# Kernel tuning notes

Measured on AMD Instinct MI355X. Metric: run time of the kernel, lower is better.

Reference implementation:

```python
import jax, jax.numpy as jnp
import numpy as np

N = 100000   # nodes
E = 600000   # edges per sign
IN = 128     # in_dim
HID = 128    # hidden_dim
H = 8        # num_heads
D = HID // H # per-head out_feats = 16
OUT = 64     # out_dim
NEG_SLOPE = 0.2


def setup_inputs() -> dict:
    key = jax.random.key(0)
    ks = jax.random.split(key, 20)
    inp = {}
    inp['features'] = jax.random.normal(ks[0], (N, IN), dtype=jnp.float32)
    inp['pos_src'] = jax.random.randint(ks[1], (E,), 0, N, dtype=jnp.int32)
    inp['pos_dst'] = jax.random.randint(ks[2], (E,), 0, N, dtype=jnp.int32)
    inp['neg_src'] = jax.random.randint(ks[3], (E,), 0, N, dtype=jnp.int32)
    inp['neg_dst'] = jax.random.randint(ks[4], (E,), 0, N, dtype=jnp.int32)
    # GATConv params (DGL: fc weight, attn_l, attn_r, bias) for pos and neg convs
    s = 0.1
    inp['W_pos'] = jax.random.normal(ks[5], (IN, H * D), dtype=jnp.float32) * s
    inp['al_pos'] = jax.random.normal(ks[6], (H, D), dtype=jnp.float32) * s
    inp['ar_pos'] = jax.random.normal(ks[7], (H, D), dtype=jnp.float32) * s
    inp['b_pos'] = jnp.zeros((H * D,), dtype=jnp.float32)
    inp['W_neg'] = jax.random.normal(ks[8], (IN, H * D), dtype=jnp.float32) * s
    inp['al_neg'] = jax.random.normal(ks[9], (H, D), dtype=jnp.float32) * s
    inp['ar_neg'] = jax.random.normal(ks[10], (H, D), dtype=jnp.float32) * s
    inp['b_neg'] = jnp.zeros((H * D,), dtype=jnp.float32)
    # final MLP: Linear(2*HID, HID) -> ReLU -> Linear(HID, OUT)
    inp['W1'] = jax.random.normal(ks[11], (2 * HID, HID), dtype=jnp.float32) * s
    inp['b1'] = jnp.zeros((HID,), dtype=jnp.float32)
    inp['W2'] = jax.random.normal(ks[12], (HID, OUT), dtype=jnp.float32) * s
    inp['b2'] = jnp.zeros((OUT,), dtype=jnp.float32)
    return inp


def gat_conv(features, src, dst, W, al, ar, b, n):
    # DGL GATConv (eval mode, no feat/attn dropout, no residual/activation)
    feat = (features @ W).reshape(n, H, D)            # [N,H,D]
    el = (feat * al).sum(-1)                          # [N,H]
    er = (feat * ar).sum(-1)                          # [N,H]
    e = jax.nn.leaky_relu(el[src] + er[dst], NEG_SLOPE)  # [E,H] per-edge logits
    # edge softmax over incoming edges of each dst node, per head
    m = jax.ops.segment_max(e, dst, num_segments=n)   # [N,H]
    ex = jnp.exp(e - m[dst])                          # [E,H]
    s = jax.ops.segment_sum(ex, dst, num_segments=n)  # [N,H]
    a = ex / s[dst]                                   # [E,H]
    rst = jax.ops.segment_sum(a[:, :, None] * feat[src], dst, num_segments=n)  # [N,H,D]
    return rst.reshape(n, H * D) + b


def reference(features, pos_src, pos_dst, neg_src, neg_dst,
              W_pos, al_pos, ar_pos, b_pos,
              W_neg, al_neg, ar_neg, b_neg,
              W1, b1, W2, b2):
    n = features.shape[0]
    h_pos = gat_conv(features, pos_src, pos_dst, W_pos, al_pos, ar_pos, b_pos, n)
    h_neg = gat_conv(features, neg_src, neg_dst, W_neg, al_neg, ar_neg, b_neg, n)
    h = jnp.concatenate([h_pos, h_neg], axis=1)       # [N, 2*HID]
    h_final = jnp.maximum(h @ W1 + b1, 0.0) @ W2 + b2  # [N, OUT]
    return (h_pos, h_neg, h_final)
```

## Files before the change

kernel.cpp:

```cpp
#include <hip/hip_runtime.h>

#define NEG_SLOPE 0.2f

typedef __attribute__((ext_vector_type(8))) short short8;
typedef __attribute__((ext_vector_type(4))) float floatx4;

__device__ __forceinline__ unsigned short f2bf(float f) {
    union { float f; unsigned u; } v; v.f = f;
    unsigned r = v.u + 0x7FFF + ((v.u >> 16) & 1);
    return (unsigned short)(r >> 16);
}
__device__ __forceinline__ float bf2f(unsigned short u) {
    return __uint_as_float(((unsigned)u) << 16);
}

__global__ void convert_w_kernel(const float* __restrict__ Wp, const float* __restrict__ Wn,
                                 const float* __restrict__ W1, const float* __restrict__ W2,
                                 unsigned short* __restrict__ Wcat, unsigned short* __restrict__ W1t,
                                 unsigned short* __restrict__ W2t) {
    int i = blockIdx.x * blockDim.x + threadIdx.x;
    if (i < 256 * 128) {
        int nr = i >> 7, k = i & 127;
        float v = (nr < 128) ? Wp[k * 128 + nr] : Wn[k * 128 + (nr - 128)];
        Wcat[i] = f2bf(v);
    } else if (i < 256 * 128 + 128 * 256) {
        int j = i - 256 * 128;
        int nr = j >> 8, k = j & 255;
        W1t[j] = f2bf(W1[k * 128 + nr]);
    } else if (i < 256 * 128 + 128 * 256 + 64 * 128) {
        int j = i - 256 * 128 - 128 * 256;
        int nr = j >> 7, k = j & 127;
        W2t[j] = f2bf(W2[k * 64 + nr]);
    }
}

template<int KDIM, int BN, bool IN_F32, bool RELU, bool OUT_BF16>
__global__ __launch_bounds__(256)
void mfma_gemm_kernel(const void* __restrict__ Av, const unsigned short* __restrict__ Wt,
                      const float* __restrict__ bias, void* __restrict__ outv, int n_rows) {
    constexpr int BM = 128, BK = 64;
    constexpr int LDA = BK + 8;
    constexpr int NT = BN / 32;
    __shared__ unsigned short As[BM * LDA];
    __shared__ unsigned short Bs[BN * LDA];
    const int tid = threadIdx.x;
    const int lane = tid & 63;
    const int wave = tid >> 6;
    const int wy = wave >> 1, wx = wave & 1;
    const int row0 = blockIdx.x * BM;
    const int n0 = blockIdx.y * BN;
    const int lrow = lane & 15;
    const int lk = (lane >> 4) * 8;

    floatx4 acc[4][NT];
#pragma unroll
    for (int mt = 0; mt < 4; mt++)
#pragma unroll
        for (int nt = 0; nt < NT; nt++) acc[mt][nt] = (floatx4){0.f, 0.f, 0.f, 0.f};

    for (int kb = 0; kb < KDIM / BK; ++kb) {
#pragma unroll
        for (int u = 0; u < 4; ++u) {
            int idx = tid + u * 256;
            int r = idx >> 3, c8 = idx & 7;
            int gr = row0 + r; if (gr >= n_rows) gr = n_rows - 1;
            if (IN_F32) {
                const float* Af = (const float*)Av + (size_t)gr * KDIM + kb * BK + c8 * 8;
                float4 va = ((const float4*)Af)[0], vb = ((const float4*)Af)[1];
                unsigned short o[8];
                o[0] = f2bf(va.x); o[1] = f2bf(va.y); o[2] = f2bf(va.z); o[3] = f2bf(va.w);
                o[4] = f2bf(vb.x); o[5] = f2bf(vb.y); o[6] = f2bf(vb.z); o[7] = f2bf(vb.w);
                *(float4*)&As[r * LDA + c8 * 8] = *(float4*)o;
            } else {
                const unsigned short* Ab = (const unsigned short*)Av;
                float4 v = *(const float4*)(Ab + (size_t)gr * KDIM + kb * BK + c8 * 8);
                *(float4*)&As[r * LDA + c8 * 8] = v;
            }
        }
#pragma unroll
        for (int u = 0; u < BN / 32; ++u) {
            int idx = tid + u * 256;
            int r = idx >> 3, c8 = idx & 7;
            float4 v = *(const float4*)(Wt + (size_t)(n0 + r) * KDIM + kb * BK + c8 * 8);
            *(float4*)&Bs[r * LDA + c8 * 8] = v;
        }
        __syncthreads();
#pragma unroll
        for (int ks = 0; ks < 2; ++ks) {
            short8 af[4], bf[NT];
#pragma unroll
            for (int mt = 0; mt < 4; ++mt)
                af[mt] = *(const short8*)&As[(wy * 64 + mt * 16 + lrow) * LDA + ks * 32 + lk];
#pragma unroll
            for (int nt = 0; nt < NT; ++nt)
                bf[nt] = *(const short8*)&Bs[(wx * (BN / 2) + nt * 16 + lrow) * LDA + ks * 32 + lk];
#pragma unroll
            for (int mt = 0; mt < 4; ++mt)
#pragma unroll
                for (int nt = 0; nt < NT; ++nt)
                    acc[mt][nt] = __builtin_amdgcn_mfma_f32_16x16x32_bf16(af[mt], bf[nt], acc[mt][nt], 0, 0, 0);
        }
        __syncthreads();
    }
    const size_t obase = (size_t)blockIdx.y * n_rows * BN;
#pragma unroll
    for (int mt = 0; mt < 4; ++mt) {
#pragma unroll
        for (int r = 0; r < 4; ++r) {
            int grow = row0 + wy * 64 + mt * 16 + (lane >> 4) * 4 + r;
            if (grow >= n_rows) continue;
#pragma unroll
            for (int nt = 0; nt < NT; ++nt) {
                int cloc = wx * (BN / 2) + nt * 16 + (lane & 15);
                float v = acc[mt][nt][r];
                if (bias) v += bias[cloc];
                if (RELU) v = fmaxf(v, 0.f);
                if (OUT_BF16) ((unsigned short*)outv)[obase + (size_t)grow * BN + cloc] = f2bf(v);
                else          ((float*)outv)[obase + (size_t)grow * BN + cloc] = v;
            }
        }
    }
}

__global__ void eler_kernel(const unsigned short* __restrict__ featb,
                            const float* __restrict__ al_p, const float* __restrict__ ar_p,
                            const float* __restrict__ al_n, const float* __restrict__ ar_n,
                            float* __restrict__ el_p, float* __restrict__ er_p,
                            float* __restrict__ el_n, float* __restrict__ er_n, int n) {
    int idx = blockIdx.x * blockDim.x + threadIdx.x;
    if (idx >= 2 * n * 8) return;
    int h = idx & 7;
    bool neg = idx >= n * 8;
    const float* al = neg ? al_n : al_p;
    const float* ar = neg ? ar_n : ar_p;
    float* el = neg ? el_n : el_p;
    float* er = neg ? er_n : er_p;
    int local = neg ? idx - n * 8 : idx;
    const unsigned* fu = (const unsigned*)(featb + (size_t)idx * 16);
    float sl = 0.f, sr = 0.f;
#pragma unroll
    for (int q = 0; q < 8; ++q) {
        unsigned u = fu[q];
        float lo = __uint_as_float(u << 16);
        float hi = __uint_as_float(u & 0xFFFF0000u);
        sl += lo * al[h * 16 + q * 2] + hi * al[h * 16 + q * 2 + 1];
        sr += lo * ar[h * 16 + q * 2] + hi * ar[h * 16 + q * 2 + 1];
    }
    el[local] = sl; er[local] = sr;
}

__global__ void count_kernel(const int* __restrict__ pos_dst, const int* __restrict__ neg_dst,
                             int* __restrict__ cnt, int ne, int npad) {
    int e = blockIdx.x * blockDim.x + threadIdx.x;
    if (e < ne) atomicAdd(&cnt[pos_dst[e]], 1);
    else if (e < 2 * ne) atomicAdd(&cnt[npad + neg_dst[e - ne]], 1);
}

__global__ __launch_bounds__(256)
void scan1_kernel(int* __restrict__ cnt, int* __restrict__ bsum) {
    __shared__ int sm[256];
    int i = blockIdx.x * 256 + threadIdx.x;
    int v = cnt[i];
    sm[threadIdx.x] = v;
    __syncthreads();
    for (int off = 1; off < 256; off <<= 1) {
        int t = (threadIdx.x >= off) ? sm[threadIdx.x - off] : 0;
        __syncthreads();
        sm[threadIdx.x] += t;
        __syncthreads();
    }
    cnt[i] = sm[threadIdx.x] - v;
    if (threadIdx.x == 255) bsum[blockIdx.x] = sm[255];
}

__global__ __launch_bounds__(512)
void scan2_kernel(int* __restrict__ bsum, int nb) {
    __shared__ int sm[512];
    int base = blockIdx.x * nb;
    int v = (threadIdx.x < nb) ? bsum[base + threadIdx.x] : 0;
    sm[threadIdx.x] = v;
    __syncthreads();
    for (int off = 1; off < 512; off <<= 1) {
        int t = (threadIdx.x >= off) ? sm[threadIdx.x - off] : 0;
        __syncthreads();
        sm[threadIdx.x] += t;
        __syncthreads();
    }
    if (threadIdx.x < nb) bsum[base + threadIdx.x] = sm[threadIdx.x] - v;
}

__global__ void scan3_kernel(int* __restrict__ cnt, const int* __restrict__ bsum,
                             int* __restrict__ offs_p, int* __restrict__ offs_n,
                             int n, int ne, int npad) {
    int i = blockIdx.x * blockDim.x + threadIdx.x;
    int v = cnt[i] + bsum[i >> 8];
    cnt[i] = v;
    if (i < n) offs_p[i] = v;
    else if (i >= npad && i - npad < n) offs_n[i - npad] = v;
    if (i == 0) { offs_p[n] = ne; offs_n[n] = ne; }
}

__global__ void scatter_kernel(const int* __restrict__ pos_src, const int* __restrict__ pos_dst,
                               const int* __restrict__ neg_src, const int* __restrict__ neg_dst,
                               int* __restrict__ cur, int* __restrict__ ssrc_p, int* __restrict__ ssrc_n,
                               int ne, int npad) {
    int e = blockIdx.x * blockDim.x + threadIdx.x;
    if (e < ne) {
        int p = atomicAdd(&cur[pos_dst[e]], 1);
        ssrc_p[p] = pos_src[e];
    } else if (e < 2 * ne) {
        int j = e - ne;
        int p = atomicAdd(&cur[npad + neg_dst[j]], 1);
        ssrc_n[p] = neg_src[j];
    }
}

__global__ __launch_bounds__(256)
void gat_gather_kernel(const int* __restrict__ offs_p, const int* __restrict__ offs_n,
                       const int* __restrict__ ssrc_p, const int* __restrict__ ssrc_n,
                       const float* __restrict__ el_p, const float* __restrict__ er_p,
                       const float* __restrict__ el_n, const float* __restrict__ er_n,
                       const unsigned short* __restrict__ featb,
                       const float* __restrict__ b_pos, const float* __restrict__ b_neg,
                       float* __restrict__ out, unsigned short* __restrict__ hcatb, int n) {
    int node = (blockIdx.x * 256 + threadIdx.x) >> 6;
    int lane = threadIdx.x & 63;
    if (node >= n) return;
    const int neg = blockIdx.y;
    const int* offs = neg ? offs_n : offs_p;
    const int* ssrc = neg ? ssrc_n : ssrc_p;
    const float* el = neg ? el_n : el_p;
    const float* er = neg ? er_n : er_p;
    const unsigned short* fb = featb + (size_t)(neg ? n : 0) * 128;
    const float* bias = neg ? b_neg : b_pos;
    float* o = out + (size_t)(neg ? n : 0) * 128;
    const int coloff = neg ? 128 : 0;

    const int h = lane >> 3;
    const float erh = er[(size_t)node * 8 + h];
    const int beg = offs[node], end = offs[node + 1];
    float acc0 = 0.f, acc1 = 0.f, denom = 0.f;

#define GSTEP(S)  do {                                                         \
        float x_ = el[(size_t)(S) * 8 + h] + erh;                              \
        x_ = x_ < 0.f ? NEG_SLOPE * x_ : x_;                                   \
        float w_ = __expf(x_);                                                 \
        denom += w_;                                                           \
        ushort2 f_ = *(const ushort2*)(fb + (size_t)(S) * 128 + lane * 2);     \
        acc0 = fmaf(w_, bf2f(f_.x), acc0);                                     \
        acc1 = fmaf(w_, bf2f(f_.y), acc1);                                     \
    } while (0)

    for (int p0 = beg; p0 < end; p0 += 64) {
        int cnt = end - p0; if (cnt > 64) cnt = 64;
        int sid = (lane < cnt) ? ssrc[p0 + lane] : 0;
        int j = 0;
        for (; j + 4 <= cnt; j += 4) {
            int s0 = __shfl(sid, j), s1 = __shfl(sid, j + 1);
            int s2 = __shfl(sid, j + 2), s3 = __shfl(sid, j + 3);
            GSTEP(s0); GSTEP(s1); GSTEP(s2); GSTEP(s3);
        }
        for (; j < cnt; ++j) {
            int s = __shfl(sid, j);
            GSTEP(s);
        }
    }
#undef GSTEP

    float inv = denom > 0.f ? 1.f / denom : 0.f;
    float2 ov;
    ov.x = fmaf(acc0, inv, bias[lane * 2]);
    ov.y = fmaf(acc1, inv, bias[lane * 2 + 1]);
    *(float2*)(o + (size_t)node * 128 + lane * 2) = ov;
    ushort2 hb; hb.x = f2bf(ov.x); hb.y = f2bf(ov.y);
    *(ushort2*)(hcatb + (size_t)node * 256 + coloff + lane * 2) = hb;
}

extern "C" void kernel_launch(void* const* d_in, const int* in_sizes, int n_in,
                              void* d_out, int out_size, void* d_ws, size_t ws_size,
                              hipStream_t stream) {
    const float* features = (const float*)d_in[0];
    const int* pos_src = (const int*)d_in[1];
    const int* pos_dst = (const int*)d_in[2];
    const int* neg_src = (const int*)d_in[3];
    const int* neg_dst = (const int*)d_in[4];
    const float* W_pos  = (const float*)d_in[5];
    const float* al_pos = (const float*)d_in[6];
    const float* ar_pos = (const float*)d_in[7];
    const float* b_pos  = (const float*)d_in[8];
    const float* W_neg  = (const float*)d_in[9];
    const float* al_neg = (const float*)d_in[10];
    const float* ar_neg = (const float*)d_in[11];
    const float* b_neg  = (const float*)d_in[12];
    const float* W1 = (const float*)d_in[13];
    const float* b1 = (const float*)d_in[14];
    const float* W2 = (const float*)d_in[15];
    const float* b2 = (const float*)d_in[16];

    const int n  = in_sizes[0] / 128;
    const int ne = in_sizes[1];
    const int nb = (n + 255) / 256;
    const int npad = nb * 256;

    float* out  = (float*)d_out;
    float* hfin = out + (size_t)n * 256;

    unsigned short* featb = (unsigned short*)d_ws;
    unsigned short* hcatb = featb + (size_t)2 * n * 128;
    unsigned short* mid   = hcatb + (size_t)n * 256;
    float* el_pos = (float*)(mid + (size_t)n * 128);
    float* er_pos = el_pos + (size_t)n * 8;
    float* el_neg = er_pos + (size_t)n * 8;
    float* er_neg = el_neg + (size_t)n * 8;
    unsigned short* Wcat = (unsigned short*)(er_neg + (size_t)n * 8);
    unsigned short* W1t  = Wcat + 256 * 128;
    unsigned short* W2t  = W1t + 128 * 256;
    int* cnt      = (int*)(W2t + 64 * 128);
    int* offs_pos = cnt + 2 * npad;
    int* offs_neg = offs_pos + (n + 1);
    int* bsum     = offs_neg + (n + 1);
    int* ssrc_pos = bsum + 2 * nb;
    int* ssrc_neg = ssrc_pos + ne;

    const int gm = (n + 127) / 128;
    const int ge2 = (2 * ne + 255) / 256;

    convert_w_kernel<<<(73728 + 255) / 256, 256, 0, stream>>>(W_pos, W_neg, W1, W2, Wcat, W1t, W2t);

    hipMemsetAsync(cnt, 0, sizeof(int) * 2 * (size_t)npad, stream);
    count_kernel<<<ge2, 256, 0, stream>>>(pos_dst, neg_dst, cnt, ne, npad);
    scan1_kernel<<<2 * nb, 256, 0, stream>>>(cnt, bsum);
    scan2_kernel<<<2, 512, 0, stream>>>(bsum, nb);
    scan3_kernel<<<2 * nb, 256, 0, stream>>>(cnt, bsum, offs_pos, offs_neg, n, ne, npad);
    scatter_kernel<<<ge2, 256, 0, stream>>>(pos_src, pos_dst, neg_src, neg_dst, cnt, ssrc_pos, ssrc_neg, ne, npad);

    mfma_gemm_kernel<128, 128, true, false, true><<<dim3(gm, 2), 256, 0, stream>>>(features, Wcat, nullptr, featb, n);

    eler_kernel<<<(2 * n * 8 + 255) / 256, 256, 0, stream>>>(featb, al_pos, ar_pos, al_neg, ar_neg,
                                                             el_pos, er_pos, el_neg, er_neg, n);

    gat_gather_kernel<<<dim3((n + 3) / 4, 2), 256, 0, stream>>>(offs_pos, offs_neg, ssrc_pos, ssrc_neg,
                                                                el_pos, er_pos, el_neg, er_neg,
                                                                featb, b_pos, b_neg, out, hcatb, n);

    mfma_gemm_kernel<256, 128, false, true, true><<<dim3(gm, 1), 256, 0, stream>>>(hcatb, W1t, b1, mid, n);
    mfma_gemm_kernel<128, 64, false, false, false><<<dim3(gm, 1), 256, 0, stream>>>(mid, W2t, b2, hfin, n);
}
```

Before: 516.1 us.

## Replace tiled MFMA GEMMs with persistent weight-resident streaming GEMM kernel

The three dense GEMMs switch from a tiled kernel that restages both A and B tiles through LDS every K-block to a persistent kernel. In the new kernel the whole weight matrix stays in swizzled LDS, and each wave streams 16-row A tiles straight from global memory into registers. The feature projection now computes both pos and neg outputs in one pass with N=256 and writes split outputs, so features are read once instead of twice. The change removes per-K-block barriers and A-tile LDS traffic, at the cost of 64KB LDS per block for the first GEMM, which limits occupancy. It also drops row-bounds handling, since ntiles = n_rows>>4 assumes n is a multiple of 16.

After: 535.6 us. +3.8%, slower.

```diff
diff --git a/kernel.cpp b/kernel.cpp
--- a/kernel.cpp
+++ b/kernel.cpp
@@ -34,89 +34,87 @@
     }
 }
 
-template<int KDIM, int BN, bool IN_F32, bool RELU, bool OUT_BF16>
+template<int KDIM, int N, bool IN_F32, bool RELU, bool OUT_BF16, bool SPLIT>
 __global__ __launch_bounds__(256)
-void mfma_gemm_kernel(const void* __restrict__ Av, const unsigned short* __restrict__ Wt,
-                      const float* __restrict__ bias, void* __restrict__ outv, int n_rows) {
-    constexpr int BM = 128, BK = 64;
-    constexpr int LDA = BK + 8;
-    constexpr int NT = BN / 32;
-    __shared__ unsigned short As[BM * LDA];
-    __shared__ unsigned short Bs[BN * LDA];
+void gemm_stream_kernel(const void* __restrict__ Av, const unsigned short* __restrict__ Wt,
+                        const float* __restrict__ bias, void* __restrict__ outv, int n_rows) {
+    constexpr int KS = KDIM / 32;
+    constexpr int NT = N / 16;
+    static_assert(N * KDIM * 2 <= 65536, "LDS budget");
+    __shared__ __align__(16) unsigned short Bs[N * KDIM];
     const int tid = threadIdx.x;
+
+    constexpr int CH = (N * KDIM) / 8;
+    for (int i = tid; i < CH; i += 256) {
+        int r = i / (KDIM / 8), c8 = i % (KDIM / 8);
+        float4 v = *(const float4*)(Wt + (size_t)r * KDIM + c8 * 8);
+        unsigned byt = ((unsigned)(r * KDIM + c8 * 8) << 1) ^ ((unsigned)(r & 7) << 4);
+        *(float4*)((char*)Bs + byt) = v;
+    }
+    __syncthreads();
+
     const int lane = tid & 63;
-    const int wave = tid >> 6;
-    const int wy = wave >> 1, wx = wave & 1;
-    const int row0 = blockIdx.x * BM;
-    const int n0 = blockIdx.y * BN;
     const int lrow = lane & 15;
-    const int lk = (lane >> 4) * 8;
-
-    floatx4 acc[4][NT];
-#pragma unroll
-    for (int mt = 0; mt < 4; mt++)
-#pragma unroll
-        for (int nt = 0; nt < NT; nt++) acc[mt][nt] = (floatx4){0.f, 0.f, 0.f, 0.f};
-
-    for (int kb = 0; kb < KDIM / BK; ++kb) {
-#pragma unroll
-        for (int u = 0; u < 4; ++u) {
-            int idx = tid + u * 256;
-            int r = idx >> 3, c8 = idx & 7;
-            int gr = row0 + r; if (gr >= n_rows) gr = n_rows - 1;
-            if (IN_F32) {
-                const float* Af = (const float*)Av + (size_t)gr * KDIM + kb * BK + c8 * 8;
-                float4 va = ((const float4*)Af)[0], vb = ((const float4*)Af)[1];
+    const int q = lane >> 4;
+    const unsigned swz = (unsigned)(lrow & 7) << 4;
+    const char* const Bsb = (const char*)Bs + lrow * (2 * KDIM);
+    const int gw = blockIdx.x * 4 + (tid >> 6);
+    const int nw = gridDim.x * 4;
+    const int ntiles = n_rows >> 4;
+
+    for (int t = gw; t < ntiles; t += nw) {
+        const int arow = t * 16 + lrow;
+        short8 af[KS];
+        if (IN_F32) {
+            const float* Af = (const float*)Av + (size_t)arow * KDIM + q * 8;
+#pragma unroll
+            for (int ks = 0; ks < KS; ++ks) {
+                float4 va = *(const float4*)(Af + ks * 32);
+                float4 vb = *(const float4*)(Af + ks * 32 + 4);
                 unsigned short o[8];
                 o[0] = f2bf(va.x); o[1] = f2bf(va.y); o[2] = f2bf(va.z); o[3] = f2bf(va.w);
                 o[4] = f2bf(vb.x); o[5] = f2bf(vb.y); o[6] = f2bf(vb.z); o[7] = f2bf(vb.w);
-                *(float4*)&As[r * LDA + c8 * 8] = *(float4*)o;
-            } else {
-                const unsigned short* Ab = (const unsigned short*)Av;
-                float4 v = *(const float4*)(Ab + (size_t)gr * KDIM + kb * BK + c8 * 8);
-                *(float4*)&As[r * LDA + c8 * 8] = v;
+                af[ks] = *(short8*)o;
             }
-        }
-#pragma unroll
-        for (int u = 0; u < BN / 32; ++u) {
-            int idx = tid + u * 256;
-            int r = idx >> 3, c8 = idx & 7;
-            float4 v = *(const float4*)(Wt + (size_t)(n0 + r) * KDIM + kb * BK + c8 * 8);
-            *(float4*)&Bs[r * LDA + c8 * 8] = v;
-        }
-        __syncthreads();
-#pragma unroll
-        for (int ks = 0; ks < 2; ++ks) {
-            short8 af[4], bf[NT];
-#pragma unroll
-            for (int mt = 0; mt < 4; ++mt)
-                af[mt] = *(const short8*)&As[(wy * 64 + mt * 16 + lrow) * LDA + ks * 32 + lk];
-#pragma unroll
-            for (int nt = 0; nt < NT; ++nt)
-                bf[nt] = *(const short8*)&Bs[(wx * (BN / 2) + nt * 16 + lrow) * LDA + ks * 32 + lk];
-#pragma unroll
-            for (int mt = 0; mt < 4; ++mt)
-#pragma unroll
-                for (int nt = 0; nt < NT; ++nt)
-                    acc[mt][nt] = __builtin_amdgcn_mfma_f32_16x16x32_bf16(af[mt], bf[nt], acc[mt][nt], 0, 0, 0);
-        }
-        __syncthreads();
-    }
-    const size_t obase = (size_t)blockIdx.y * n_rows * BN;
-#pragma unroll
-    for (int mt = 0; mt < 4; ++mt) {
-#pragma unroll
-        for (int r = 0; r < 4; ++r) {
-            int grow = row0 + wy * 64 + mt * 16 + (lane >> 4) * 4 + r;
-            if (grow >= n_rows) continue;
+        } else {
+            const unsigned short* Ab = (const unsigned short*)Av + (size_t)arow * KDIM + q * 8;
+#pragma unroll
+            for (int ks = 0; ks < KS; ++ks)
+                af[ks] = *(const short8*)(Ab + ks * 32);
+        }
+
+        floatx4 acc[NT];
+#pragma unroll
+        for (int nt = 0; nt < NT; ++nt) acc[nt] = (floatx4){0.f, 0.f, 0.f, 0.f};
+
+#pragma unroll
+        for (int ks = 0; ks < KS; ++ks) {
+            const char* bp = Bsb + (((unsigned)(ks * 64 + q * 16)) ^ swz);
 #pragma unroll
             for (int nt = 0; nt < NT; ++nt) {
-                int cloc = wx * (BN / 2) + nt * 16 + (lane & 15);
-                float v = acc[mt][nt][r];
-                if (bias) v += bias[cloc];
+                short8 bf = *(const short8*)(bp + nt * (16 * 2 * KDIM));
+                acc[nt] = __builtin_amdgcn_mfma_f32_16x16x32_bf16(af[ks], bf, acc[nt], 0, 0, 0);
+            }
+        }
+
+#pragma unroll
+        for (int nt = 0; nt < NT; ++nt) {
+            const int cl = nt * 16 + lrow;
+            const float bv = bias ? bias[cl] : 0.f;
+#pragma unroll
+            for (int r = 0; r < 4; ++r) {
+                const int grow = t * 16 + q * 4 + r;
+                float v = acc[nt][r] + bv;
                 if (RELU) v = fmaxf(v, 0.f);
-                if (OUT_BF16) ((unsigned short*)outv)[obase + (size_t)grow * BN + cloc] = f2bf(v);
-                else          ((float*)outv)[obase + (size_t)grow * BN + cloc] = v;
+                if (SPLIT) {
+                    unsigned short* op = (unsigned short*)outv +
+                        ((nt >= NT / 2) ? (size_t)n_rows * (N / 2) : (size_t)0);
+                    op[(size_t)grow * (N / 2) + (cl & (N / 2 - 1))] = f2bf(v);
+                } else if (OUT_BF16) {
+                    ((unsigned short*)outv)[(size_t)grow * N + cl] = f2bf(v);
+                } else {
+                    ((float*)outv)[(size_t)grow * N + cl] = v;
+                }
             }
         }
     }
@@ -322,7 +320,6 @@
     int* ssrc_pos = bsum + 2 * nb;
     int* ssrc_neg = ssrc_pos + ne;
 
-    const int gm = (n + 127) / 128;
     const int ge2 = (2 * ne + 255) / 256;
 
     convert_w_kernel<<<(73728 + 255) / 256, 256, 0, stream>>>(W_pos, W_neg, W1, W2, Wcat, W1t, W2t);
@@ -334,7 +331,8 @@
     scan3_kernel<<<2 * nb, 256, 0, stream>>>(cnt, bsum, offs_pos, offs_neg, n, ne, npad);
     scatter_kernel<<<ge2, 256, 0, stream>>>(pos_src, pos_dst, neg_src, neg_dst, cnt, ssrc_pos, ssrc_neg, ne, npad);
 
-    mfma_gemm_kernel<128, 128, true, false, true><<<dim3(gm, 2), 256, 0, stream>>>(features, Wcat, nullptr, featb, n);
+    gemm_stream_kernel<128, 256, true, false, true, true>
+        <<<512, 256, 0, stream>>>(features, Wcat, nullptr, featb, n);
 
     eler_kernel<<<(2 * n * 8 + 255) / 256, 256, 0, stream>>>(featb, al_pos, ar_pos, al_neg, ar_neg,
                                                              el_pos, er_pos, el_neg, er_neg, n);
@@ -343,6 +341,8 @@
                                                                 el_pos, er_pos, el_neg, er_neg,
                                                                 featb, b_pos, b_neg, out, hcatb, n);
 
-    mfma_gemm_kernel<256, 128, false, true, true><<<dim3(gm, 1), 256, 0, stream>>>(hcatb, W1t, b1, mid, n);
-    mfma_gemm_kernel<128, 64, false, false, false><<<dim3(gm, 1), 256, 0, stream>>>(mid, W2t, b2, hfin, n);
-}
+    gemm_stream_kernel<256, 128, false, true, true, false>
+        <<<512, 256, 0, stream>>>(hcatb, W1t, b1, mid, n);
+    gemm_stream_kernel<128, 64, false, false, false, false>
+        <<<512, 256, 0, stream>>>(mid, W2t, b2, hfin, n);
+}
```
